# Kernel tuning notes

Hardware: AMD Instinct MI355X
Metric: run time of the kernel (lower is better)

## Reference

```python
import jax, jax.numpy as jnp
import numpy as np

EMB = 768
HEADS = 8
HEAD_DIM = EMB // HEADS  # 96
B, N = 4, 2048


def setup_inputs() -> dict:
    key = jax.random.key(0)
    ks = jax.random.split(key, 9)
    s = 1.0 / np.sqrt(EMB)
    x = jax.random.normal(ks[0], (B, N, EMB), dtype=jnp.float32)
    Wq = jax.random.uniform(ks[1], (EMB, EMB), jnp.float32, -s, s)
    bq = jax.random.uniform(ks[2], (EMB,), jnp.float32, -s, s)
    Wk = jax.random.uniform(ks[3], (EMB, EMB), jnp.float32, -s, s)
    bk = jax.random.uniform(ks[4], (EMB,), jnp.float32, -s, s)
    Wv = jax.random.uniform(ks[5], (EMB, EMB), jnp.float32, -s, s)
    bv = jax.random.uniform(ks[6], (EMB,), jnp.float32, -s, s)
    Wo = jax.random.uniform(ks[7], (EMB, EMB), jnp.float32, -s, s)
    bo = jax.random.uniform(ks[8], (EMB,), jnp.float32, -s, s)
    return {"x": x, "Wq": Wq, "bq": bq, "Wk": Wk, "bk": bk,
            "Wv": Wv, "bv": bv, "Wo": Wo, "bo": bo}


def _split_heads(t):
    b, n, _ = t.shape
    return t.reshape(b, n, HEADS, HEAD_DIM).transpose(0, 2, 1, 3)  # b h n d


def reference(x, Wq, bq, Wk, bk, Wv, bv, Wo, bo):
    q = _split_heads(x @ Wq + bq)
    k = _split_heads(x @ Wk + bk)
    v = _split_heads(x @ Wv + bv)
    # NOTE: faithful to source — softmax on UNSCALED logits, then divide by sqrt(head_dim)
    energy = jnp.einsum('bhqd,bhkd->bhqk', q, k)
    att = jax.nn.softmax(energy, axis=-1) / np.sqrt(HEAD_DIM)
    out = jnp.einsum('bhqk,bhkd->bhqd', att, v)
    out = out.transpose(0, 2, 1, 3).reshape(x.shape[0], x.shape[1], EMB)
    return out @ Wo + bo
```

## Files before the change

kernel.cpp:

```cpp
#include <hip/hip_runtime.h>

typedef _Float16 half_t;
typedef __attribute__((ext_vector_type(8))) _Float16 half8;
typedef __attribute__((ext_vector_type(2))) __fp16 fp16x2;
typedef __attribute__((ext_vector_type(4))) float f32x4;
typedef __attribute__((ext_vector_type(16))) float f32x16;

#define EMB 768
#define HEADS 8
#define HD 96
#define BB 4
#define NN 2048
#define BN (BB*NN)

static __device__ __forceinline__ f32x4 mfma16(half8 a, half8 b, f32x4 c) {
    return __builtin_amdgcn_mfma_f32_16x16x32_f16(a, b, c, 0, 0, 0);
}
static __device__ __forceinline__ f32x16 mfma32(half8 a, half8 b, f32x16 c) {
    return __builtin_amdgcn_mfma_f32_32x32x16_f16(a, b, c, 0, 0, 0);
}
static __device__ __forceinline__ unsigned pkrtz(float a, float b) {
    fp16x2 h = __builtin_amdgcn_cvt_pkrtz(a, b);
    return __builtin_bit_cast(unsigned, h);
}
static __device__ __forceinline__ unsigned sx32(unsigned v) {
    return (unsigned)__shfl_xor((int)v, 32);
}
static __device__ __forceinline__ half8 pack8(float4 a, float4 b) {
    union { unsigned u[4]; half8 h; } t;
    t.u[0] = pkrtz(a.x, a.y); t.u[1] = pkrtz(a.z, a.w);
    t.u[2] = pkrtz(b.x, b.y); t.u[3] = pkrtz(b.z, b.w);
    return t.h;
}

__global__ __launch_bounds__(256) void cvt_transpose_w(
    const float* __restrict__ W0, const float* __restrict__ W1,
    const float* __restrict__ W2, const float* __restrict__ W3,
    half_t* __restrict__ T0, half_t* __restrict__ T1,
    half_t* __restrict__ T2, half_t* __restrict__ T3)
{
    const float* W; half_t* T;
    switch (blockIdx.z) {
        case 0: W = W0; T = T0; break;
        case 1: W = W1; T = T1; break;
        case 2: W = W2; T = T2; break;
        default: W = W3; T = T3; break;
    }
    __shared__ float ls[32][33];
    const int k0 = blockIdx.x * 32, n0 = blockIdx.y * 32;
    const int r = threadIdx.x >> 3, c4 = (threadIdx.x & 7) * 4;
    float4 v = *(const float4*)&W[(size_t)(k0 + r) * EMB + n0 + c4];
    ls[r][c4+0] = v.x; ls[r][c4+1] = v.y; ls[r][c4+2] = v.z; ls[r][c4+3] = v.w;
    __syncthreads();
    union { half_t h[4]; uint2 u; } t;
    #pragma unroll
    for (int j = 0; j < 4; ++j) t.h[j] = (half_t)ls[c4 + j][r];
    *(uint2*)&T[(size_t)(n0 + r) * EMB + k0 + c4] = t.u;
}

__global__ __launch_bounds__(256) void proj_qkv_h(
    const float* __restrict__ x,
    const half_t* __restrict__ WqT, const float* __restrict__ bq,
    const half_t* __restrict__ WkT, const float* __restrict__ bk,
    const half_t* __restrict__ WvT, const float* __restrict__ bv,
    half_t* __restrict__ Qo, half_t* __restrict__ Ko, half_t* __restrict__ Vt)
{
    const half_t* WT; const float* bias;
    const int z = blockIdx.z;
    if (z == 0)      { WT = WqT; bias = bq; }
    else if (z == 1) { WT = WkT; bias = bk; }
    else             { WT = WvT; bias = bv; }

    __shared__ half_t As[128][56];
    __shared__ half_t Bs[128][56];

    const int tid = threadIdx.x;
    const int lane = tid & 63;
    const int wid = tid >> 6;
    const int lr = lane & 15;
    const int lkg = lane >> 4;
    const int wm = (wid >> 1) * 64;
    const int wn = (wid & 1) * 64;
    const int mbase = blockIdx.x * 128;
    const int nbase = blockIdx.y * 128;

    const int srr = tid >> 2;
    const int skk = (tid & 3) * 8;

    f32x4 acc[4][4];
    const f32x4 z4 = {0.f, 0.f, 0.f, 0.f};
    #pragma unroll
    for (int i = 0; i < 4; ++i)
        #pragma unroll
        for (int j = 0; j < 4; ++j) acc[i][j] = z4;

    const float*  aptr = x  + (size_t)(mbase + srr) * EMB + skk;
    const half_t* bptr = WT + (size_t)(nbase + srr) * EMB + skk;

    half8 a0 = pack8(*(const float4*)(aptr),
                     *(const float4*)(aptr + 4));
    half8 a1 = pack8(*(const float4*)(aptr + 64 * EMB),
                     *(const float4*)(aptr + 64 * EMB + 4));
    half8 b0 = *(const half8*)bptr;
    half8 b1 = *(const half8*)(bptr + 64 * EMB);

    for (int k0 = 0; k0 < EMB; k0 += 32) {
        __syncthreads();
        *(half8*)&As[srr][skk]      = a0;
        *(half8*)&As[srr + 64][skk] = a1;
        *(half8*)&Bs[srr][skk]      = b0;
        *(half8*)&Bs[srr + 64][skk] = b1;
        __syncthreads();
        if (k0 + 32 < EMB) {
            a0 = pack8(*(const float4*)(aptr + k0 + 32),
                       *(const float4*)(aptr + k0 + 36));
            a1 = pack8(*(const float4*)(aptr + k0 + 32 + 64 * EMB),
                       *(const float4*)(aptr + k0 + 36 + 64 * EMB));
            b0 = *(const half8*)(bptr + k0 + 32);
            b1 = *(const half8*)(bptr + k0 + 32 + 64 * EMB);
        }
        half8 af[4], bf[4];
        #pragma unroll
        for (int mi = 0; mi < 4; ++mi)
            af[mi] = *(const half8*)&As[wm + mi*16 + lr][lkg*8];
        #pragma unroll
        for (int ni = 0; ni < 4; ++ni)
            bf[ni] = *(const half8*)&Bs[wn + ni*16 + lr][lkg*8];
        #pragma unroll
        for (int mi = 0; mi < 4; ++mi)
            #pragma unroll
            for (int ni = 0; ni < 4; ++ni)
                acc[mi][ni] = mfma16(af[mi], bf[ni], acc[mi][ni]);
    }

    const float qscale = (z == 0) ? 1.4426950408889634f : 1.0f;

    #pragma unroll
    for (int ni = 0; ni < 4; ++ni) {
        const int e = nbase + wn + ni*16 + lr;
        const float be = bias[e];
        const int h = e / HD, d = e % HD;
        #pragma unroll
        for (int mi = 0; mi < 4; ++mi) {
            const int row0 = mbase + wm + mi*16 + lkg*4;
            const int b = row0 >> 11, n0 = row0 & (NN - 1);
            if (z == 2) {
                union { half_t hh[4]; uint2 u; } t;
                #pragma unroll
                for (int r = 0; r < 4; ++r) t.hh[r] = (half_t)(acc[mi][ni][r] + be);
                *(uint2*)&Vt[((size_t)(b*HEADS + h) * HD + d) * NN + n0] = t.u;
            } else {
                half_t* outp = (z == 0) ? Qo : Ko;
                #pragma unroll
                for (int r = 0; r < 4; ++r)
                    outp[((size_t)(b*HEADS + h) * NN + n0 + r) * HD + d] =
                        (half_t)((acc[mi][ni][r] + be) * qscale);
            }
        }
    }
}

__global__ __launch_bounds__(256, 3) void attn_h(
    const half_t* __restrict__ Qh, const half_t* __restrict__ Kh,
    const half_t* __restrict__ Vth, half_t* __restrict__ AOh)
{
    __shared__ __align__(16) char smem[25088];

    const int tid = threadIdx.x;
    const int lane = tid & 63;
    const int wid = tid >> 6;
    const int l31 = lane & 31;
    const int b5 = lane >> 5;
    const int qsub = wid & 1;
    const int sub = wid >> 1;
    const int qbase = blockIdx.x * 64;
    const int bh = blockIdx.y;

    const half_t* Qp = Qh + (size_t)bh * NN * HD;
    const half_t* Kp = Kh + (size_t)bh * NN * HD;
    const half_t* Vp = Vth + (size_t)bh * HD * NN;
    half_t* AOp = AOh + (size_t)bh * NN * HD;

    const int kr = tid >> 2;
    const int kcb = (tid & 3) * 48;
    const int vd = tid >> 1;
    const int vcb = (tid & 1) * 64;
    half8 kv0, kv1, kv2, vv0, vv1, vv2, vv3;
    {
        const half_t* ksrc = Kp + (size_t)kr * HD + kcb / 2;
        kv0 = *(const half8*)(ksrc);
        kv1 = *(const half8*)(ksrc + 8);
        kv2 = *(const half8*)(ksrc + 16);
        if (tid < 192) {
            const half_t* vsrc = Vp + (size_t)vd * NN + vcb / 2;
            vv0 = *(const half8*)(vsrc);      vv1 = *(const half8*)(vsrc + 8);
            vv2 = *(const half8*)(vsrc + 16); vv3 = *(const half8*)(vsrc + 24);
        }
    }

    {
        const int r = tid >> 2;
        const int cb = (tid & 3) * 48;
        const half_t* src = Qp + (size_t)(qbase + r) * HD + cb / 2;
        #pragma unroll
        for (int c = 0; c < 3; ++c) {
            half8 q = *(const half8*)(src + c * 8);
            *(half8*)(smem + ((r * 192 + cb + c * 16) ^ ((r & 7) << 4))) = q;
        }
    }
    __syncthreads();
    half8 qf[6];
    {
        const int r = qsub * 32 + l31;
        #pragma unroll
        for (int kg = 0; kg < 6; ++kg)
            qf[kg] = *(const half8*)(smem + ((r * 192 + kg * 32 + 16 * b5) ^ ((r & 7) << 4)));
    }
    __syncthreads();

    f32x16 acc[3];
    const f32x16 z16 = {0.f,0.f,0.f,0.f,0.f,0.f,0.f,0.f,0.f,0.f,0.f,0.f,0.f,0.f,0.f,0.f};
    acc[0] = z16; acc[1] = z16; acc[2] = z16;
    float mreg = -1e30f, lreg = 0.f;

    const int kvrow = sub * 32 + l31;

    for (int kt = 0; kt < NN / 64; ++kt) {
        *(half8*)(smem + ((kr * 192 + kcb +  0) ^ ((kr & 7) << 4))) = kv0;
        *(half8*)(smem + ((kr * 192 + kcb + 16) ^ ((kr & 7) << 4))) = kv1;
        *(half8*)(smem + ((kr * 192 + kcb + 32) ^ ((kr & 7) << 4))) = kv2;
        if (tid < 192) {
            char* vb = smem + 12288;
            *(half8*)(vb + ((vd * 128 + vcb +  0) ^ ((vd & 7) << 4))) = vv0;
            *(half8*)(vb + ((vd * 128 + vcb + 16) ^ ((vd & 7) << 4))) = vv1;
            *(half8*)(vb + ((vd * 128 + vcb + 32) ^ ((vd & 7) << 4))) = vv2;
            *(half8*)(vb + ((vd * 128 + vcb + 48) ^ ((vd & 7) << 4))) = vv3;
        }
        __syncthreads();

        if (kt + 1 < NN / 64) {
            const int kb = (kt + 1) * 64;
            const half_t* ksrc = Kp + (size_t)(kb + kr) * HD + kcb / 2;
            kv0 = *(const half8*)(ksrc);
            kv1 = *(const half8*)(ksrc + 8);
            kv2 = *(const half8*)(ksrc + 16);
            if (tid < 192) {
                const half_t* vsrc = Vp + (size_t)vd * NN + kb + vcb / 2;
                vv0 = *(const half8*)(vsrc);      vv1 = *(const half8*)(vsrc + 8);
                vv2 = *(const half8*)(vsrc + 16); vv3 = *(const half8*)(vsrc + 24);
            }
        }

        f32x16 st = z16;
        #pragma unroll
        for (int kg = 0; kg < 6; ++kg) {
            half8 kf = *(const half8*)(smem +
                ((kvrow * 192 + kg * 32 + 16 * b5) ^ ((kvrow & 7) << 4)));
            st = mfma32(kf, qf[kg], st);
        }

        float tm = st[0];
        #pragma unroll
        for (int i = 1; i < 16; ++i) tm = fmaxf(tm, st[i]);
        tm = fmaxf(tm, __shfl_xor(tm, 32));

        if (!__all(tm <= mreg + 8.0f)) {
            const float mn = fmaxf(mreg, tm);
            const float sc = exp2f(mreg - mn);
            lreg *= sc;
            #pragma unroll
            for (int db = 0; db < 3; ++db)
                #pragma unroll
                for (int i = 0; i < 16; ++i) acc[db][i] *= sc;
            mreg = mn;
        }

        float rs = 0.f;
        #pragma unroll
        for (int i = 0; i < 16; ++i) {
            const float p = exp2f(st[i] - mreg);
            st[i] = p;
            rs += p;
        }
        rs += __shfl_xor(rs, 32);
        lreg += rs;

        unsigned pk[4][2];
        #pragma unroll
        for (int rr = 0; rr < 4; ++rr) {
            pk[rr][0] = pkrtz(st[rr*4+0], st[rr*4+1]);
            pk[rr][1] = pkrtz(st[rr*4+2], st[rr*4+3]);
        }

        #pragma unroll
        for (int ks = 0; ks < 2; ++ks) {
            const unsigned z0 = b5 ? pk[2*ks][0] : pk[2*ks+1][0];
            const unsigned z1 = b5 ? pk[2*ks][1] : pk[2*ks+1][1];
            const unsigned x0 = sx32(z0);
            const unsigned x1 = sx32(z1);
            union { unsigned u[4]; half8 h; } afu;
            afu.u[0] = b5 ? x0 : pk[2*ks][0];
            afu.u[1] = b5 ? x1 : pk[2*ks][1];
            afu.u[2] = b5 ? pk[2*ks+1][0] : x0;
            afu.u[3] = b5 ? pk[2*ks+1][1] : x1;
            const half8 af = afu.h;
            #pragma unroll
            for (int db = 0; db < 3; ++db) {
                const int d = db * 32 + l31;
                half8 vf = *(const half8*)(smem + 12288 +
                    ((d * 128 + sub * 64 + ks * 32 + 16 * b5) ^ ((d & 7) << 4)));
                acc[db] = mfma32(vf, af, acc[db]);
            }
        }
        __syncthreads();
    }

    float* fb = (float*)smem;
    fb[tid] = mreg;
    fb[256 + tid] = lreg;
    __syncthreads();
    const float mp = fb[tid ^ 128];
    const float lp = fb[256 + (tid ^ 128)];
    const float mc = fmaxf(mreg, mp);
    const float sc = exp2f(mreg - mc);
    const float lc = lreg * sc + lp * exp2f(mp - mc);
    __syncthreads();
    if (wid >= 2) {
        float* rec = fb + (qsub * 64 + lane) * 49;
        #pragma unroll
        for (int db = 0; db < 3; ++db)
            #pragma unroll
            for (int i = 0; i < 16; ++i) rec[db*16 + i] = acc[db][i] * sc;
    }
    __syncthreads();
    if (wid < 2) {
        const float* rec = fb + (qsub * 64 + lane) * 49;
        const float isq = 0.10206207261596577f;
        const float inv = isq / lc;
        const int q = qbase + qsub * 32 + l31;
        half_t* dst = AOp + (size_t)q * HD;
        #pragma unroll
        for (int db = 0; db < 3; ++db)
            #pragma unroll
            for (int rr = 0; rr < 4; ++rr) {
                const int d0 = db * 32 + rr * 8 + 4 * b5;
                union { half_t h[4]; uint2 u; } t;
                #pragma unroll
                for (int r = 0; r < 4; ++r)
                    t.h[r] = (half_t)((acc[db][rr*4 + r] * sc + rec[db*16 + rr*4 + r]) * inv);
                *(uint2*)&dst[d0] = t.u;
            }
    }
}

__global__ __launch_bounds__(256) void proj_out_h(
    const half_t* __restrict__ AOh, const half_t* __restrict__ WoT,
    const float* __restrict__ bo, float* __restrict__ out)
{
    __shared__ half_t As[128][56];
    __shared__ half_t Bs[128][56];

    const int tid = threadIdx.x;
    const int lane = tid & 63;
    const int wid = tid >> 6;
    const int lr = lane & 15;
    const int lkg = lane >> 4;
    const int wm = (wid >> 1) * 64;
    const int wn = (wid & 1) * 64;
    const int mbase = blockIdx.x * 128;
    const int nbase = blockIdx.y * 128;

    const int srr = tid >> 2;
    const int skk = (tid & 3) * 8;

    const int arow0 = mbase + srr;
    const int ab0 = arow0 >> 11, an0 = arow0 & (NN - 1);
    const int arow1 = arow0 + 64;
    const int ab1 = arow1 >> 11, an1 = arow1 & (NN - 1);

    f32x4 acc[4][4];
    const f32x4 z4 = {0.f, 0.f, 0.f, 0.f};
    #pragma unroll
    for (int i = 0; i < 4; ++i)
        #pragma unroll
        for (int j = 0; j < 4; ++j) acc[i][j] = z4;

    const half_t* bptr = WoT + (size_t)(nbase + srr) * EMB + skk;

#define ALOAD(b_, n_, k0_) \
    (*(const half8*)&AOh[((size_t)((b_)*HEADS + (k0_)/HD) * NN + (n_)) * HD + ((k0_)%HD) + skk])

    half8 a0 = ALOAD(ab0, an0, 0);
    half8 a1 = ALOAD(ab1, an1, 0);
    half8 b0 = *(const half8*)bptr;
    half8 b1 = *(const half8*)(bptr + 64 * EMB);

    for (int k0 = 0; k0 < EMB; k0 += 32) {
        __syncthreads();
        *(half8*)&As[srr][skk]      = a0;
        *(half8*)&As[srr + 64][skk] = a1;
        *(half8*)&Bs[srr][skk]      = b0;
        *(half8*)&Bs[srr + 64][skk] = b1;
        __syncthreads();
        if (k0 + 32 < EMB) {
            const int kn = k0 + 32;
            a0 = ALOAD(ab0, an0, kn);
            a1 = ALOAD(ab1, an1, kn);
            b0 = *(const half8*)(bptr + kn);
            b1 = *(const half8*)(bptr + kn + 64 * EMB);
        }
        half8 af[4], bf[4];
        #pragma unroll
        for (int mi = 0; mi < 4; ++mi)
            af[mi] = *(const half8*)&As[wm + mi*16 + lr][lkg*8];
        #pragma unroll
        for (int ni = 0; ni < 4; ++ni)
            bf[ni] = *(const half8*)&Bs[wn + ni*16 + lr][lkg*8];
        #pragma unroll
        for (int mi = 0; mi < 4; ++mi)
            #pragma unroll
            for (int ni = 0; ni < 4; ++ni)
                acc[mi][ni] = mfma16(af[mi], bf[ni], acc[mi][ni]);
    }
#undef ALOAD

    #pragma unroll
    for (int ni = 0; ni < 4; ++ni) {
        const int e = nbase + wn + ni*16 + lr;
        const float be = bo[e];
        #pragma unroll
        for (int mi = 0; mi < 4; ++mi) {
            const int row0 = mbase + wm + mi*16 + lkg*4;
            #pragma unroll
            for (int r = 0; r < 4; ++r)
                out[(size_t)(row0 + r) * EMB + e] = acc[mi][ni][r] + be;
        }
    }
}

extern "C" void kernel_launch(void* const* d_in, const int* in_sizes, int n_in,
                              void* d_out, int out_size, void* d_ws, size_t ws_size,
                              hipStream_t stream)
{
    const float* x  = (const float*)d_in[0];
    const float* Wq = (const float*)d_in[1];
    const float* bq = (const float*)d_in[2];
    const float* Wk = (const float*)d_in[3];
    const float* bk = (const float*)d_in[4];
    const float* Wv = (const float*)d_in[5];
    const float* bv = (const float*)d_in[6];
    const float* Wo = (const float*)d_in[7];
    const float* bo = (const float*)d_in[8];

    const size_t SZ = (size_t)BN * EMB;
    const size_t WS = (size_t)EMB * EMB;

    half_t* ws  = (half_t*)d_ws;
    half_t* WqT = ws;
    half_t* WkT = WqT + WS;
    half_t* WvT = WkT + WS;
    half_t* WoT = WvT + WS;
    half_t* Qh  = WoT + WS;
    half_t* Kh  = Qh  + SZ;
    half_t* Vth = Kh  + SZ;
    half_t* AOh = Vth + SZ;

    cvt_transpose_w<<<dim3(EMB/32, EMB/32, 4), 256, 0, stream>>>(
        Wq, Wk, Wv, Wo, WqT, WkT, WvT, WoT);

    proj_qkv_h<<<dim3(BN/128, EMB/128, 3), 256, 0, stream>>>(
        x, WqT, bq, WkT, bk, WvT, bv, Qh, Kh, Vth);

    attn_h<<<dim3(NN/64, BB*HEADS), 256, 0, stream>>>(Qh, Kh, Vth, AOh);

    proj_out_h<<<dim3(BN/128, EMB/128), 256, 0, stream>>>(AOh, WoT, bo, (float*)d_out);
}
```

Before: 167.8 us.

## Load K/V fragments straight from global into registers, drop LDS staging

The attention kernel stops staging K and V tiles through shared memory with block-wide barriers. Each wave now loads its own MFMA K and V fragments directly from global memory into registers, double-buffered across two key tiles, and Q fragments are also read directly. The grid is flattened and remapped so neighbouring blocks cover different heads of the same batch, and the occupancy hint drops from 3 to 2 blocks per SU to make room for the extra registers. This removes LDS writes and reads and the per-tile syncthreads, at the cost of more register pressure and less-coalesced global loads that depend on L2 reuse.

Measured after the change: 209.2 us. 24.7% more time.

```diff
diff --git a/kernel.cpp b/kernel.cpp
--- a/kernel.cpp
+++ b/kernel.cpp
@@ -160,7 +160,7 @@
     }
 }
 
-__global__ __launch_bounds__(256, 3) void attn_h(
+__global__ __launch_bounds__(256, 2) void attn_h(
     const half_t* __restrict__ Qh, const half_t* __restrict__ Kh,
     const half_t* __restrict__ Vth, half_t* __restrict__ AOh)
 {
@@ -173,147 +173,109 @@
     const int b5 = lane >> 5;
     const int qsub = wid & 1;
     const int sub = wid >> 1;
-    const int qbase = blockIdx.x * 64;
-    const int bh = blockIdx.y;
+
+    const int f = blockIdx.x;
+    const int bh = (f & 7) + 8 * (f >> 8);
+    const int qbase = ((f >> 3) & 31) * 64;
 
     const half_t* Qp = Qh + (size_t)bh * NN * HD;
     const half_t* Kp = Kh + (size_t)bh * NN * HD;
     const half_t* Vp = Vth + (size_t)bh * HD * NN;
     half_t* AOp = AOh + (size_t)bh * NN * HD;
 
-    const int kr = tid >> 2;
-    const int kcb = (tid & 3) * 48;
-    const int vd = tid >> 1;
-    const int vcb = (tid & 1) * 64;
-    half8 kv0, kv1, kv2, vv0, vv1, vv2, vv3;
-    {
-        const half_t* ksrc = Kp + (size_t)kr * HD + kcb / 2;
-        kv0 = *(const half8*)(ksrc);
-        kv1 = *(const half8*)(ksrc + 8);
-        kv2 = *(const half8*)(ksrc + 16);
-        if (tid < 192) {
-            const half_t* vsrc = Vp + (size_t)vd * NN + vcb / 2;
-            vv0 = *(const half8*)(vsrc);      vv1 = *(const half8*)(vsrc + 8);
-            vv2 = *(const half8*)(vsrc + 16); vv3 = *(const half8*)(vsrc + 24);
-        }
-    }
-
-    {
-        const int r = tid >> 2;
-        const int cb = (tid & 3) * 48;
-        const half_t* src = Qp + (size_t)(qbase + r) * HD + cb / 2;
-        #pragma unroll
-        for (int c = 0; c < 3; ++c) {
-            half8 q = *(const half8*)(src + c * 8);
-            *(half8*)(smem + ((r * 192 + cb + c * 16) ^ ((r & 7) << 4))) = q;
-        }
-    }
-    __syncthreads();
+    const int qrow = qbase + qsub * 32 + l31;
     half8 qf[6];
-    {
-        const int r = qsub * 32 + l31;
-        #pragma unroll
-        for (int kg = 0; kg < 6; ++kg)
-            qf[kg] = *(const half8*)(smem + ((r * 192 + kg * 32 + 16 * b5) ^ ((r & 7) << 4)));
-    }
-    __syncthreads();
-
+    #pragma unroll
+    for (int kg = 0; kg < 6; ++kg)
+        qf[kg] = *(const half8*)&Qp[(size_t)qrow * HD + kg * 16 + b5 * 8];
+
+    const half_t* kbase = Kp + (size_t)(sub * 32 + l31) * HD + b5 * 8;
+    const half_t* vbase = Vp + (size_t)l31 * NN + sub * 32 + b5 * 8;
+
+#define KLOAD(DST, KT)                                                        \
+    {   const half_t* p_ = kbase + (size_t)(KT) * (64 * HD);                  \
+        _Pragma("unroll")                                                     \
+        for (int kg = 0; kg < 6; ++kg)                                        \
+            DST[kg] = *(const half8*)(p_ + kg * 16); }
+
+#define VLOAD(DST, KT)                                                        \
+    {   const half_t* p_ = vbase + (size_t)(KT) * 64;                         \
+        _Pragma("unroll")                                                     \
+        for (int db = 0; db < 3; ++db)                                        \
+            _Pragma("unroll")                                                 \
+            for (int ks = 0; ks < 2; ++ks)                                    \
+                DST[db*2+ks] = *(const half8*)(p_ + (size_t)db*32*NN + ks*16); }
+
+#define ATTN_STEP(KF, VF)                                                     \
+    {   f32x16 st = z16;                                                      \
+        _Pragma("unroll")                                                     \
+        for (int kg = 0; kg < 6; ++kg) st = mfma32(KF[kg], qf[kg], st);       \
+        float tm = st[0];                                                     \
+        _Pragma("unroll")                                                     \
+        for (int i = 1; i < 16; ++i) tm = fmaxf(tm, st[i]);                   \
+        tm = fmaxf(tm, __shfl_xor(tm, 32));                                   \
+        if (!__all(tm <= mreg + 8.0f)) {                                      \
+            const float mn = fmaxf(mreg, tm);                                 \
+            const float sc = exp2f(mreg - mn);                                \
+            lreg *= sc;                                                       \
+            _Pragma("unroll")                                                 \
+            for (int db = 0; db < 3; ++db)                                    \
+                _Pragma("unroll")                                             \
+                for (int i = 0; i < 16; ++i) acc[db][i] *= sc;                \
+            mreg = mn;                                                        \
+        }                                                                     \
+        float rs = 0.f;                                                       \
+        _Pragma("unroll")                                                     \
+        for (int i = 0; i < 16; ++i) {                                        \
+            const float p = exp2f(st[i] - mreg);                              \
+            st[i] = p; rs += p;                                               \
+        }                                                                     \
+        rs += __shfl_xor(rs, 32);                                             \
+        lreg += rs;                                                           \
+        unsigned pk[4][2];                                                    \
+        _Pragma("unroll")                                                     \
+        for (int rr = 0; rr < 4; ++rr) {                                      \
+            pk[rr][0] = pkrtz(st[rr*4+0], st[rr*4+1]);                        \
+            pk[rr][1] = pkrtz(st[rr*4+2], st[rr*4+3]);                        \
+        }                                                                     \
+        _Pragma("unroll")                                                     \
+        for (int ks = 0; ks < 2; ++ks) {                                      \
+            const unsigned z0 = b5 ? pk[2*ks][0] : pk[2*ks+1][0];             \
+            const unsigned z1 = b5 ? pk[2*ks][1] : pk[2*ks+1][1];             \
+            const unsigned x0 = sx32(z0);                                     \
+            const unsigned x1 = sx32(z1);                                     \
+            union { unsigned u[4]; half8 h; } afu;                            \
+            afu.u[0] = b5 ? x0 : pk[2*ks][0];                                 \
+            afu.u[1] = b5 ? x1 : pk[2*ks][1];                                 \
+            afu.u[2] = b5 ? pk[2*ks+1][0] : x0;                               \
+            afu.u[3] = b5 ? pk[2*ks+1][1] : x1;                               \
+            const half8 af = afu.h;                                           \
+            _Pragma("unroll")                                                 \
+            for (int db = 0; db < 3; ++db)                                    \
+                acc[db] = mfma32(VF[db*2+ks], af, acc[db]);                   \
+        }                                                                     \
+    }
+
+    const f32x16 z16 = {0.f,0.f,0.f,0.f,0.f,0.f,0.f,0.f,0.f,0.f,0.f,0.f,0.f,0.f,0.f,0.f};
     f32x16 acc[3];
-    const f32x16 z16 = {0.f,0.f,0.f,0.f,0.f,0.f,0.f,0.f,0.f,0.f,0.f,0.f,0.f,0.f,0.f,0.f};
     acc[0] = z16; acc[1] = z16; acc[2] = z16;
     float mreg = -1e30f, lreg = 0.f;
 
-    const int kvrow = sub * 32 + l31;
-
-    for (int kt = 0; kt < NN / 64; ++kt) {
-        *(half8*)(smem + ((kr * 192 + kcb +  0) ^ ((kr & 7) << 4))) = kv0;
-        *(half8*)(smem + ((kr * 192 + kcb + 16) ^ ((kr & 7) << 4))) = kv1;
-        *(half8*)(smem + ((kr * 192 + kcb + 32) ^ ((kr & 7) << 4))) = kv2;
-        if (tid < 192) {
-            char* vb = smem + 12288;
-            *(half8*)(vb + ((vd * 128 + vcb +  0) ^ ((vd & 7) << 4))) = vv0;
-            *(half8*)(vb + ((vd * 128 + vcb + 16) ^ ((vd & 7) << 4))) = vv1;
-            *(half8*)(vb + ((vd * 128 + vcb + 32) ^ ((vd & 7) << 4))) = vv2;
-            *(half8*)(vb + ((vd * 128 + vcb + 48) ^ ((vd & 7) << 4))) = vv3;
-        }
-        __syncthreads();
-
-        if (kt + 1 < NN / 64) {
-            const int kb = (kt + 1) * 64;
-            const half_t* ksrc = Kp + (size_t)(kb + kr) * HD + kcb / 2;
-            kv0 = *(const half8*)(ksrc);
-            kv1 = *(const half8*)(ksrc + 8);
-            kv2 = *(const half8*)(ksrc + 16);
-            if (tid < 192) {
-                const half_t* vsrc = Vp + (size_t)vd * NN + kb + vcb / 2;
-                vv0 = *(const half8*)(vsrc);      vv1 = *(const half8*)(vsrc + 8);
-                vv2 = *(const half8*)(vsrc + 16); vv3 = *(const half8*)(vsrc + 24);
-            }
-        }
-
-        f32x16 st = z16;
-        #pragma unroll
-        for (int kg = 0; kg < 6; ++kg) {
-            half8 kf = *(const half8*)(smem +
-                ((kvrow * 192 + kg * 32 + 16 * b5) ^ ((kvrow & 7) << 4)));
-            st = mfma32(kf, qf[kg], st);
-        }
-
-        float tm = st[0];
-        #pragma unroll
-        for (int i = 1; i < 16; ++i) tm = fmaxf(tm, st[i]);
-        tm = fmaxf(tm, __shfl_xor(tm, 32));
-
-        if (!__all(tm <= mreg + 8.0f)) {
-            const float mn = fmaxf(mreg, tm);
-            const float sc = exp2f(mreg - mn);
-            lreg *= sc;
-            #pragma unroll
-            for (int db = 0; db < 3; ++db)
-                #pragma unroll
-                for (int i = 0; i < 16; ++i) acc[db][i] *= sc;
-            mreg = mn;
-        }
-
-        float rs = 0.f;
-        #pragma unroll
-        for (int i = 0; i < 16; ++i) {
-            const float p = exp2f(st[i] - mreg);
-            st[i] = p;
-            rs += p;
-        }
-        rs += __shfl_xor(rs, 32);
-        lreg += rs;
-
-        unsigned pk[4][2];
-        #pragma unroll
-        for (int rr = 0; rr < 4; ++rr) {
-            pk[rr][0] = pkrtz(st[rr*4+0], st[rr*4+1]);
-            pk[rr][1] = pkrtz(st[rr*4+2], st[rr*4+3]);
-        }
-
-        #pragma unroll
-        for (int ks = 0; ks < 2; ++ks) {
-            const unsigned z0 = b5 ? pk[2*ks][0] : pk[2*ks+1][0];
-            const unsigned z1 = b5 ? pk[2*ks][1] : pk[2*ks+1][1];
-            const unsigned x0 = sx32(z0);
-            const unsigned x1 = sx32(z1);
-            union { unsigned u[4]; half8 h; } afu;
-            afu.u[0] = b5 ? x0 : pk[2*ks][0];
-            afu.u[1] = b5 ? x1 : pk[2*ks][1];
-            afu.u[2] = b5 ? pk[2*ks+1][0] : x0;
-            afu.u[3] = b5 ? pk[2*ks+1][1] : x1;
-            const half8 af = afu.h;
-            #pragma unroll
-            for (int db = 0; db < 3; ++db) {
-                const int d = db * 32 + l31;
-                half8 vf = *(const half8*)(smem + 12288 +
-                    ((d * 128 + sub * 64 + ks * 32 + 16 * b5) ^ ((d & 7) << 4)));
-                acc[db] = mfma32(vf, af, acc[db]);
-            }
-        }
-        __syncthreads();
-    }
+    half8 kA[6], kB[6], vf[6];
+    KLOAD(kA, 0);
+
+    for (int kt = 0; kt < NN / 64; kt += 2) {
+        VLOAD(vf, kt);
+        KLOAD(kB, kt + 1);
+        ATTN_STEP(kA, vf);
+        VLOAD(vf, kt + 1);
+        if (kt + 2 < NN / 64) KLOAD(kA, kt + 2);
+        ATTN_STEP(kB, vf);
+    }
+
+#undef KLOAD
+#undef VLOAD
+#undef ATTN_STEP
 
     float* fb = (float*)smem;
     fb[tid] = mreg;
@@ -337,8 +299,7 @@
         const float* rec = fb + (qsub * 64 + lane) * 49;
         const float isq = 0.10206207261596577f;
         const float inv = isq / lc;
-        const int q = qbase + qsub * 32 + l31;
-        half_t* dst = AOp + (size_t)q * HD;
+        half_t* dst = AOp + (size_t)qrow * HD;
         #pragma unroll
         for (int db = 0; db < 3; ++db)
             #pragma unroll
@@ -471,7 +432,7 @@
     proj_qkv_h<<<dim3(BN/128, EMB/128, 3), 256, 0, stream>>>(
         x, WqT, bq, WkT, bk, WvT, bv, Qh, Kh, Vth);
 
-    attn_h<<<dim3(NN/64, BB*HEADS), 256, 0, stream>>>(Qh, Kh, Vth, AOh);
+    attn_h<<<dim3((NN/64) * (BB*HEADS)), 256, 0, stream>>>(Qh, Kh, Vth, AOh);
 
     proj_out_h<<<dim3(BN/128, EMB/128), 256, 0, stream>>>(AOh, WoT, bo, (float*)d_out);
 }
```

## Double-buffer K/V tiles in attention, remap blocks, add MFMA priority hints

Applied to the files above, without the earlier changes.

Splits the attention kernel's shared memory into two K/V buffers so the next tile is written into the alternate buffer after compute, which removes one barrier per iteration. It also flattens the grid to 1D and remaps block indices so consecutive blocks cover different heads, likely to spread KV traffic across caches. It brackets the MFMA loops with s_setprio and rewrites the row-max reduction with three-input max. The doubled LDS (48KB) may reduce occupancy below the launch_bounds target of 3 blocks, and the max rewrite leaves a dead redundant shuffle computation.

Result: no change. 168.5 us (+0.4%).

```diff
diff --git a/kernel.cpp b/kernel.cpp
--- a/kernel.cpp
+++ b/kernel.cpp
@@ -25,6 +25,9 @@
 }
 static __device__ __forceinline__ unsigned sx32(unsigned v) {
     return (unsigned)__shfl_xor((int)v, 32);
+}
+static __device__ __forceinline__ float max3f(float a, float b, float c) {
+    return fmaxf(fmaxf(a, b), c);
 }
 static __device__ __forceinline__ half8 pack8(float4 a, float4 b) {
     union { unsigned u[4]; half8 h; } t;
@@ -164,7 +167,7 @@
     const half_t* __restrict__ Qh, const half_t* __restrict__ Kh,
     const half_t* __restrict__ Vth, half_t* __restrict__ AOh)
 {
-    __shared__ __align__(16) char smem[25088];
+    __shared__ __align__(16) char smem[49152];
 
     const int tid = threadIdx.x;
     const int lane = tid & 63;
@@ -173,8 +176,10 @@
     const int b5 = lane >> 5;
     const int qsub = wid & 1;
     const int sub = wid >> 1;
-    const int qbase = blockIdx.x * 64;
-    const int bh = blockIdx.y;
+
+    const int f = blockIdx.x;
+    const int bh = (f & 7) + 8 * (f >> 8);
+    const int qbase = ((f >> 3) & 31) * 64;
 
     const half_t* Qp = Qh + (size_t)bh * NN * HD;
     const half_t* Kp = Kh + (size_t)bh * NN * HD;
@@ -185,18 +190,33 @@
     const int kcb = (tid & 3) * 48;
     const int vd = tid >> 1;
     const int vcb = (tid & 1) * 64;
-    half8 kv0, kv1, kv2, vv0, vv1, vv2, vv3;
-    {
-        const half_t* ksrc = Kp + (size_t)kr * HD + kcb / 2;
-        kv0 = *(const half8*)(ksrc);
-        kv1 = *(const half8*)(ksrc + 8);
-        kv2 = *(const half8*)(ksrc + 16);
-        if (tid < 192) {
-            const half_t* vsrc = Vp + (size_t)vd * NN + vcb / 2;
-            vv0 = *(const half8*)(vsrc);      vv1 = *(const half8*)(vsrc + 8);
-            vv2 = *(const half8*)(vsrc + 16); vv3 = *(const half8*)(vsrc + 24);
-        }
-    }
+
+    half8 kva, kvb, kvc, vv0, vv1, vv2, vv3;
+
+#define KGLOAD(KT) {                                                          \
+        const half_t* ksrc_ = Kp + (size_t)((KT) * 64 + kr) * HD + kcb / 2;   \
+        kva = *(const half8*)(ksrc_);                                         \
+        kvb = *(const half8*)(ksrc_ + 8);                                     \
+        kvc = *(const half8*)(ksrc_ + 16); }
+#define VGLOAD(KT) if (tid < 192) {                                           \
+        const half_t* vsrc_ = Vp + (size_t)vd * NN + (KT) * 64 + vcb / 2;     \
+        vv0 = *(const half8*)(vsrc_);      vv1 = *(const half8*)(vsrc_ + 8);  \
+        vv2 = *(const half8*)(vsrc_ + 16); vv3 = *(const half8*)(vsrc_ + 24); }
+#define WRITEBUF(BASE) {                                                      \
+        char* kb_ = (BASE);                                                   \
+        *(half8*)(kb_ + ((kr * 192 + kcb +  0) ^ ((kr & 7) << 4))) = kva;     \
+        *(half8*)(kb_ + ((kr * 192 + kcb + 16) ^ ((kr & 7) << 4))) = kvb;     \
+        *(half8*)(kb_ + ((kr * 192 + kcb + 32) ^ ((kr & 7) << 4))) = kvc;     \
+        if (tid < 192) {                                                      \
+            char* vb_ = (BASE) + 12288;                                       \
+            *(half8*)(vb_ + ((vd * 128 + vcb +  0) ^ ((vd & 7) << 4))) = vv0; \
+            *(half8*)(vb_ + ((vd * 128 + vcb + 16) ^ ((vd & 7) << 4))) = vv1; \
+            *(half8*)(vb_ + ((vd * 128 + vcb + 32) ^ ((vd & 7) << 4))) = vv2; \
+            *(half8*)(vb_ + ((vd * 128 + vcb + 48) ^ ((vd & 7) << 4))) = vv3; \
+        } }
+
+    KGLOAD(0);
+    VGLOAD(0);
 
     {
         const int r = tid >> 2;
@@ -218,6 +238,8 @@
     }
     __syncthreads();
 
+    WRITEBUF(smem);
+
     f32x16 acc[3];
     const f32x16 z16 = {0.f,0.f,0.f,0.f,0.f,0.f,0.f,0.f,0.f,0.f,0.f,0.f,0.f,0.f,0.f,0.f};
     acc[0] = z16; acc[1] = z16; acc[2] = z16;
@@ -226,43 +248,37 @@
     const int kvrow = sub * 32 + l31;
 
     for (int kt = 0; kt < NN / 64; ++kt) {
-        *(half8*)(smem + ((kr * 192 + kcb +  0) ^ ((kr & 7) << 4))) = kv0;
-        *(half8*)(smem + ((kr * 192 + kcb + 16) ^ ((kr & 7) << 4))) = kv1;
-        *(half8*)(smem + ((kr * 192 + kcb + 32) ^ ((kr & 7) << 4))) = kv2;
-        if (tid < 192) {
-            char* vb = smem + 12288;
-            *(half8*)(vb + ((vd * 128 + vcb +  0) ^ ((vd & 7) << 4))) = vv0;
-            *(half8*)(vb + ((vd * 128 + vcb + 16) ^ ((vd & 7) << 4))) = vv1;
-            *(half8*)(vb + ((vd * 128 + vcb + 32) ^ ((vd & 7) << 4))) = vv2;
-            *(half8*)(vb + ((vd * 128 + vcb + 48) ^ ((vd & 7) << 4))) = vv3;
-        }
         __syncthreads();
 
         if (kt + 1 < NN / 64) {
-            const int kb = (kt + 1) * 64;
-            const half_t* ksrc = Kp + (size_t)(kb + kr) * HD + kcb / 2;
-            kv0 = *(const half8*)(ksrc);
-            kv1 = *(const half8*)(ksrc + 8);
-            kv2 = *(const half8*)(ksrc + 16);
-            if (tid < 192) {
-                const half_t* vsrc = Vp + (size_t)vd * NN + kb + vcb / 2;
-                vv0 = *(const half8*)(vsrc);      vv1 = *(const half8*)(vsrc + 8);
-                vv2 = *(const half8*)(vsrc + 16); vv3 = *(const half8*)(vsrc + 24);
-            }
-        }
+            KGLOAD(kt + 1);
+            VGLOAD(kt + 1);
+        }
+
+        const char* kb = smem + (kt & 1) * 24576;
+        const char* vb = kb + 12288;
 
         f32x16 st = z16;
+        __builtin_amdgcn_s_setprio(1);
         #pragma unroll
         for (int kg = 0; kg < 6; ++kg) {
-            half8 kf = *(const half8*)(smem +
+            half8 kf = *(const half8*)(kb +
                 ((kvrow * 192 + kg * 32 + 16 * b5) ^ ((kvrow & 7) << 4)));
             st = mfma32(kf, qf[kg], st);
         }
-
-        float tm = st[0];
-        #pragma unroll
-        for (int i = 1; i < 16; ++i) tm = fmaxf(tm, st[i]);
-        tm = fmaxf(tm, __shfl_xor(tm, 32));
+        __builtin_amdgcn_s_setprio(0);
+
+        float t0 = max3f(st[0],  st[1],  st[2]);
+        float t1 = max3f(st[3],  st[4],  st[5]);
+        float t2 = max3f(st[6],  st[7],  st[8]);
+        float t3 = max3f(st[9],  st[10], st[11]);
+        float t4 = max3f(st[12], st[13], st[14]);
+        float tm = max3f(max3f(t0, t1, t2), max3f(t3, t4, st[15]),
+                         __shfl_xor(max3f(max3f(t0, t1, t2), t3, st[15]), 32));
+        {
+            float tml = max3f(max3f(t0, t1, t2), max3f(t3, t4, st[15]), -1e30f);
+            tm = fmaxf(tml, __shfl_xor(tml, 32));
+        }
 
         if (!__all(tm <= mreg + 8.0f)) {
             const float mn = fmaxf(mreg, tm);
@@ -304,16 +320,25 @@
             afu.u[2] = b5 ? pk[2*ks+1][0] : x0;
             afu.u[3] = b5 ? pk[2*ks+1][1] : x1;
             const half8 af = afu.h;
+            __builtin_amdgcn_s_setprio(1);
             #pragma unroll
             for (int db = 0; db < 3; ++db) {
                 const int d = db * 32 + l31;
-                half8 vf = *(const half8*)(smem + 12288 +
+                half8 vf = *(const half8*)(vb +
                     ((d * 128 + sub * 64 + ks * 32 + 16 * b5) ^ ((d & 7) << 4)));
                 acc[db] = mfma32(vf, af, acc[db]);
             }
-        }
-        __syncthreads();
-    }
+            __builtin_amdgcn_s_setprio(0);
+        }
+
+        if (kt + 1 < NN / 64) {
+            WRITEBUF(smem + ((kt + 1) & 1) * 24576);
+        }
+    }
+
+#undef KGLOAD
+#undef VGLOAD
+#undef WRITEBUF
 
     float* fb = (float*)smem;
     fb[tid] = mreg;
@@ -471,7 +496,7 @@
     proj_qkv_h<<<dim3(BN/128, EMB/128, 3), 256, 0, stream>>>(
         x, WqT, bq, WkT, bk, WvT, bv, Qh, Kh, Vth);
 
-    attn_h<<<dim3(NN/64, BB*HEADS), 256, 0, stream>>>(Qh, Kh, Vth, AOh);
+    attn_h<<<dim3((NN/64) * (BB*HEADS)), 256, 0, stream>>>(Qh, Kh, Vth, AOh);
 
     proj_out_h<<<dim3(BN/128, EMB/128), 256, 0, stream>>>(AOh, WoT, bo, (float*)d_out);
 }
```
